# Optimization experiments

Hardware: AMD Instinct MI355X
Metric: run time of the kernel (lower is better)

The kernel has to match this reference:

```python
import jax, jax.numpy as jnp
import numpy as np

K_TOP = 2  # top-k experts per token (MoE k)


def setup_inputs() -> dict:
    key = jax.random.key(0)
    ks = jax.random.split(key, 4)
    B, D, H, E = 4096, 1024, 2048, 8
    x = jax.random.normal(ks[0], (B, D), dtype=jnp.float32)
    w_gate = jax.random.normal(ks[1], (D, E), dtype=jnp.float32) * 0.02
    W1 = jax.random.normal(ks[2], (E, D, H), dtype=jnp.float32) * (1.0 / np.sqrt(D))
    b1 = jnp.zeros((E, H), dtype=jnp.float32)
    W2 = jax.random.normal(ks[3], (E, H, D), dtype=jnp.float32) * (1.0 / np.sqrt(H))
    b2 = jnp.zeros((E, D), dtype=jnp.float32)
    return {"x": x, "w_gate": w_gate, "W1": W1, "b1": b1, "W2": W2, "b2": b2}


def _top_k_gates(logits, k):
    # noisy_top_k_gating, eval path (noisy_gating=False / train=False):
    # softmax over the top-k logits, scattered back to [B, E]; other gates are 0.
    B, E = logits.shape
    top_logits, top_idx = jax.lax.top_k(logits, k)       # [B, k]
    top_gates = jax.nn.softmax(top_logits, axis=-1)      # [B, k]
    rows = jnp.arange(B)[:, None]
    gates = jnp.zeros((B, E), dtype=logits.dtype).at[rows, top_idx].set(top_gates)
    return gates


def reference(x, w_gate, W1, b1, W2, b2):
    # Gating
    logits = x @ w_gate                                  # [B, E]
    gates = _top_k_gates(logits, K_TOP)                  # [B, E], sparse (top-k nonzero)
    # Experts: MLP(fc1 -> relu -> fc2) per expert. Dense-all-experts form is
    # mathematically identical to dispatch/combine since zero gates contribute 0.
    h = jax.nn.relu(jnp.einsum('bd,edh->beh', x, W1) + b1[None])   # [B, E, H]
    y = jnp.einsum('beh,ehd->bed', h, W2) + b2[None]               # [B, E, D]
    out = jnp.einsum('be,bed->bd', gates, y)                       # gated scatter-combine
    return out
```

## Files before the change

kernel.cpp:

```cpp
#include <hip/hip_runtime.h>

#define B_TOK 4096
#define DDIM  1024
#define HDIM  2048
#define NEXP  8
#define MAXTOK 4096
#define BM 128
#define BN 128
#define BK 32

#define OFF_W1T  0ull
#define OFF_W2T  33554432ull
#define OFF_XB   67108864ull
#define OFF_H    75497472ull
#define OFF_Y    109051904ull
#define OFF_TOK  125829120ull
#define OFF_GATE 125960192ull
#define OFF_PAIR 126091264ull
#define OFF_CNT  126124032ull
#define OFF_OFFS 126124096ull
#define OFF_EIDX (OFF_Y)
#define OFF_GCO  (OFF_Y + 16384ull)

typedef __attribute__((ext_vector_type(4))) float f32x4;
typedef __attribute__((ext_vector_type(8))) short bf16x8;

static __device__ __forceinline__ unsigned short f2bf(float f) {
    unsigned u = __builtin_bit_cast(unsigned, f);
    unsigned r = (u + 0x7FFFu + ((u >> 16) & 1u)) >> 16;
    return (unsigned short)r;
}
static __device__ __forceinline__ float bf2f(unsigned short s) {
    unsigned u = ((unsigned)s) << 16;
    return __builtin_bit_cast(float, u);
}

#define AS1(p) ((const __attribute__((address_space(1))) void*)(p))
#define AS3(p) ((__attribute__((address_space(3))) void*)(p))

__global__ void __launch_bounds__(256) gating_logits_kernel(
    const float* __restrict__ x, const float* __restrict__ wg,
    int* __restrict__ eidx, float* __restrict__ gco) {
    int wave = threadIdx.x >> 6;
    int lane = threadIdx.x & 63;
    int b = blockIdx.x * 4 + wave;
    float acc[NEXP];
#pragma unroll
    for (int e = 0; e < NEXP; e++) acc[e] = 0.f;
    const float* xr = x + (size_t)b * DDIM;
#pragma unroll
    for (int i = 0; i < DDIM / 64; i++) {
        int d = i * 64 + lane;
        float xv = xr[d];
        const float4* wrow = (const float4*)(wg + (size_t)d * NEXP);
        float4 w0 = wrow[0], w1 = wrow[1];
        acc[0] += xv * w0.x; acc[1] += xv * w0.y; acc[2] += xv * w0.z; acc[3] += xv * w0.w;
        acc[4] += xv * w1.x; acc[5] += xv * w1.y; acc[6] += xv * w1.z; acc[7] += xv * w1.w;
    }
#pragma unroll
    for (int off = 32; off >= 1; off >>= 1)
#pragma unroll
        for (int e = 0; e < NEXP; e++) acc[e] += __shfl_xor(acc[e], off);
    if (lane == 0) {
        int i1 = 0; float m1 = acc[0];
        for (int e = 1; e < NEXP; e++) if (acc[e] > m1) { m1 = acc[e]; i1 = e; }
        int i2 = (i1 == 0) ? 1 : 0; float m2 = -1e30f;
        for (int e = 0; e < NEXP; e++) { if (e == i1) continue; if (acc[e] > m2) { m2 = acc[e]; i2 = e; } }
        float g1 = 1.f / (1.f + expf(m2 - m1));
        eidx[b] = i1 | (i2 << 16);
        gco[b] = g1;
    }
}

__global__ void __launch_bounds__(256) build_kernel(
    const int* __restrict__ eidx, const float* __restrict__ gco,
    int* __restrict__ counts, int* __restrict__ tok,
    float* __restrict__ gate, int* __restrict__ pair) {
    __shared__ int lhist[NEXP];
    __shared__ int gbase[NEXP];
    int t = threadIdx.x;
    if (t < NEXP) lhist[t] = 0;
    __syncthreads();
    int b = blockIdx.x * 256 + t;
    int ep = eidx[b];
    int e1 = ep & 0xffff, e2 = ep >> 16;
    float g1 = gco[b], g2 = 1.f - g1;
    int l1 = atomicAdd(&lhist[e1], 1);
    int l2 = atomicAdd(&lhist[e2], 1);
    __syncthreads();
    if (t < NEXP) gbase[t] = atomicAdd(&counts[t], lhist[t]);
    __syncthreads();
    int s1 = gbase[e1] + l1, s2 = gbase[e2] + l2;
    tok[e1 * MAXTOK + s1] = b; gate[e1 * MAXTOK + s1] = g1; pair[b * 2 + 0] = e1 * MAXTOK + s1;
    tok[e2 * MAXTOK + s2] = b; gate[e2 * MAXTOK + s2] = g2; pair[b * 2 + 1] = e2 * MAXTOK + s2;
}

__global__ void scan_kernel(const int* __restrict__ counts, int* __restrict__ offs) {
    if (threadIdx.x == 0) {
        int s = 0;
        for (int e = 0; e < NEXP; e++) { offs[e] = s; s += counts[e]; }
    }
}

__global__ void __launch_bounds__(256) cvtx_kernel(const float* __restrict__ src, short* __restrict__ dst) {
    int i = blockIdx.x * 256 + threadIdx.x;
    float4 v = ((const float4*)src)[i];
    short4 o;
    o.x = (short)f2bf(v.x); o.y = (short)f2bf(v.y);
    o.z = (short)f2bf(v.z); o.w = (short)f2bf(v.w);
    ((short4*)dst)[i] = o;
}

__global__ void __launch_bounds__(256) tcvt_kernel(const float* __restrict__ src, short* __restrict__ dst,
                                                   int R, int C) {
    __shared__ float tile[64][65];
    int e = blockIdx.z;
    size_t base = (size_t)e * R * C;
    int r0 = blockIdx.y * 64, c0 = blockIdx.x * 64;
    int t = threadIdx.x;
    int rr = t >> 4, c4 = (t & 15) * 4;
    const float* s = src + base + (size_t)r0 * C + c0;
#pragma unroll
    for (int i = 0; i < 4; i++) {
        float4 v = *(const float4*)(s + (size_t)(rr + i * 16) * C + c4);
        tile[rr + i * 16][c4 + 0] = v.x; tile[rr + i * 16][c4 + 1] = v.y;
        tile[rr + i * 16][c4 + 2] = v.z; tile[rr + i * 16][c4 + 3] = v.w;
    }
    __syncthreads();
    short* d = dst + base + (size_t)c0 * R + r0;
    int hr0 = t >> 4, dc = (t & 15) * 4;
#pragma unroll
    for (int i = 0; i < 4; i++) {
        int hr = hr0 + i * 16;
        short4 o;
        o.x = (short)f2bf(tile[dc + 0][hr]); o.y = (short)f2bf(tile[dc + 1][hr]);
        o.z = (short)f2bf(tile[dc + 2][hr]); o.w = (short)f2bf(tile[dc + 3][hr]);
        *(short4*)(d + (size_t)hr * R + dc) = o;
    }
}

__global__ void __launch_bounds__(256) fc1_kernel(
    const short* __restrict__ Xb, const short* __restrict__ W1T, const float* __restrict__ b1,
    short* __restrict__ h, const int* __restrict__ tok,
    const int* __restrict__ counts, const int* __restrict__ offs) {
    int e = blockIdx.z;
    int cnt = counts[e];
    int m0 = blockIdx.y * BM;
    if (m0 >= cnt) return;
    int n0 = blockIdx.x * BN;
    int baseh = offs[e];

    __shared__ short As[BM * BK];
    __shared__ short Bs[BN * BK];

    int t = threadIdx.x;
    int wave = t >> 6, lane = t & 63;

    const short* asrc[2]; short* adst[2];
    const short* bsrc[2]; short* bdst[2];
#pragma unroll
    for (int i = 0; i < 2; i++) {
        int e0 = wave * 512 + i * 2048 + lane * 8;
        int r = e0 >> 5, ck = e0 & 31;
        int trow = m0 + r;
        int tid2 = (trow < cnt) ? tok[e * MAXTOK + trow] : 0;
        asrc[i] = Xb + (size_t)tid2 * DDIM + ck;
        adst[i] = As + wave * 512 + i * 2048;
        bsrc[i] = W1T + ((size_t)e * HDIM + n0 + r) * DDIM + ck;
        bdst[i] = Bs + wave * 512 + i * 2048;
    }

    int wr = (wave >> 1) * 64, wc = (wave & 1) * 64;
    f32x4 acc[4][4];
    f32x4 zero = {0.f, 0.f, 0.f, 0.f};
#pragma unroll
    for (int m = 0; m < 4; m++)
#pragma unroll
        for (int n = 0; n < 4; n++) acc[m][n] = zero;

    int aoff[4], boff[4];
#pragma unroll
    for (int m = 0; m < 4; m++) aoff[m] = (wr + m * 16 + (lane & 15)) * BK + (lane >> 4) * 8;
#pragma unroll
    for (int n = 0; n < 4; n++) boff[n] = (wc + n * 16 + (lane & 15)) * BK + (lane >> 4) * 8;

    for (int kt = 0; kt < DDIM / BK; kt++) {
        int k0 = kt * BK;
        __builtin_amdgcn_global_load_lds(AS1(asrc[0] + k0), AS3(adst[0]), 16, 0, 0);
        __builtin_amdgcn_global_load_lds(AS1(asrc[1] + k0), AS3(adst[1]), 16, 0, 0);
        __builtin_amdgcn_global_load_lds(AS1(bsrc[0] + k0), AS3(bdst[0]), 16, 0, 0);
        __builtin_amdgcn_global_load_lds(AS1(bsrc[1] + k0), AS3(bdst[1]), 16, 0, 0);
        __syncthreads();
        bf16x8 af[4], bg[4];
#pragma unroll
        for (int m = 0; m < 4; m++) af[m] = *(const bf16x8*)(As + aoff[m]);
#pragma unroll
        for (int n = 0; n < 4; n++) bg[n] = *(const bf16x8*)(Bs + boff[n]);
#pragma unroll
        for (int m = 0; m < 4; m++)
#pragma unroll
            for (int n = 0; n < 4; n++)
                acc[m][n] = __builtin_amdgcn_mfma_f32_16x16x32_bf16(af[m], bg[n], acc[m][n], 0, 0, 0);
        __syncthreads();
    }

#pragma unroll
    for (int n = 0; n < 4; n++) {
        int col = n0 + wc + n * 16 + (lane & 15);
        float bias = b1[e * HDIM + col];
#pragma unroll
        for (int m = 0; m < 4; m++) {
            int rbase = wr + m * 16 + (lane >> 4) * 4;
#pragma unroll
            for (int j = 0; j < 4; j++) {
                int r = rbase + j;
                if (m0 + r < cnt) {
                    float v = acc[m][n][j] + bias;
                    v = v > 0.f ? v : 0.f;
                    h[(size_t)(baseh + m0 + r) * HDIM + col] = (short)f2bf(v);
                }
            }
        }
    }
}

__global__ void __launch_bounds__(256) fc2_kernel(
    const short* __restrict__ h, const short* __restrict__ W2T, const float* __restrict__ b2,
    short* __restrict__ ybuf, const int* __restrict__ counts, const int* __restrict__ offs) {
    int e = blockIdx.z;
    int cnt = counts[e];
    int m0 = blockIdx.y * BM;
    if (m0 >= cnt) return;
    int n0 = blockIdx.x * BN;
    int baseh = offs[e];

    __shared__ short As[BM * BK];
    __shared__ short Bs[BN * BK];

    int t = threadIdx.x;
    int wave = t >> 6, lane = t & 63;

    const short* asrc[2]; short* adst[2];
    const short* bsrc[2]; short* bdst[2];
#pragma unroll
    for (int i = 0; i < 2; i++) {
        int e0 = wave * 512 + i * 2048 + lane * 8;
        int r = e0 >> 5, ck = e0 & 31;
        asrc[i] = h + (size_t)(baseh + m0 + r) * HDIM + ck;
        adst[i] = As + wave * 512 + i * 2048;
        bsrc[i] = W2T + ((size_t)e * DDIM + n0 + r) * HDIM + ck;
        bdst[i] = Bs + wave * 512 + i * 2048;
    }

    int wr = (wave >> 1) * 64, wc = (wave & 1) * 64;
    f32x4 acc[4][4];
    f32x4 zero = {0.f, 0.f, 0.f, 0.f};
#pragma unroll
    for (int m = 0; m < 4; m++)
#pragma unroll
        for (int n = 0; n < 4; n++) acc[m][n] = zero;

    int aoff[4], boff[4];
#pragma unroll
    for (int m = 0; m < 4; m++) aoff[m] = (wr + m * 16 + (lane & 15)) * BK + (lane >> 4) * 8;
#pragma unroll
    for (int n = 0; n < 4; n++) boff[n] = (wc + n * 16 + (lane & 15)) * BK + (lane >> 4) * 8;

    for (int kt = 0; kt < HDIM / BK; kt++) {
        int k0 = kt * BK;
        __builtin_amdgcn_global_load_lds(AS1(asrc[0] + k0), AS3(adst[0]), 16, 0, 0);
        __builtin_amdgcn_global_load_lds(AS1(asrc[1] + k0), AS3(adst[1]), 16, 0, 0);
        __builtin_amdgcn_global_load_lds(AS1(bsrc[0] + k0), AS3(bdst[0]), 16, 0, 0);
        __builtin_amdgcn_global_load_lds(AS1(bsrc[1] + k0), AS3(bdst[1]), 16, 0, 0);
        __syncthreads();
        bf16x8 af[4], bg[4];
#pragma unroll
        for (int m = 0; m < 4; m++) af[m] = *(const bf16x8*)(As + aoff[m]);
#pragma unroll
        for (int n = 0; n < 4; n++) bg[n] = *(const bf16x8*)(Bs + boff[n]);
#pragma unroll
        for (int m = 0; m < 4; m++)
#pragma unroll
            for (int n = 0; n < 4; n++)
                acc[m][n] = __builtin_amdgcn_mfma_f32_16x16x32_bf16(af[m], bg[n], acc[m][n], 0, 0, 0);
        __syncthreads();
    }

#pragma unroll
    for (int n = 0; n < 4; n++) {
        int col = n0 + wc + n * 16 + (lane & 15);
        float bias = b2[e * DDIM + col];
#pragma unroll
        for (int m = 0; m < 4; m++) {
            int rbase = wr + m * 16 + (lane >> 4) * 4;
#pragma unroll
            for (int j = 0; j < 4; j++) {
                int r = rbase + j;
                if (m0 + r < cnt) {
                    float v = acc[m][n][j] + bias;
                    ybuf[(size_t)(baseh + m0 + r) * DDIM + col] = (short)f2bf(v);
                }
            }
        }
    }
}

__global__ void __launch_bounds__(256) combine_kernel(
    const short* __restrict__ ybuf, const float* __restrict__ gate,
    const int* __restrict__ pair, const int* __restrict__ offs, float* __restrict__ out) {
    int b = blockIdx.x;
    int p0 = pair[b * 2], p1 = pair[b * 2 + 1];
    float g0 = gate[p0], g1 = gate[p1];
    int r0 = offs[p0 >> 12] + (p0 & 4095);
    int r1 = offs[p1 >> 12] + (p1 & 4095);
    const short4* y0 = (const short4*)(ybuf + (size_t)r0 * DDIM);
    const short4* y1 = (const short4*)(ybuf + (size_t)r1 * DDIM);
    float4* o = (float4*)(out + (size_t)b * DDIM);
    int t = threadIdx.x;
    short4 a = y0[t], c = y1[t];
    float4 v;
    v.x = g0 * bf2f((unsigned short)a.x) + g1 * bf2f((unsigned short)c.x);
    v.y = g0 * bf2f((unsigned short)a.y) + g1 * bf2f((unsigned short)c.y);
    v.z = g0 * bf2f((unsigned short)a.z) + g1 * bf2f((unsigned short)c.z);
    v.w = g0 * bf2f((unsigned short)a.w) + g1 * bf2f((unsigned short)c.w);
    o[t] = v;
}

extern "C" void kernel_launch(void* const* d_in, const int* in_sizes, int n_in,
                              void* d_out, int out_size, void* d_ws, size_t ws_size,
                              hipStream_t stream) {
    const float* x  = (const float*)d_in[0];
    const float* wg = (const float*)d_in[1];
    const float* W1 = (const float*)d_in[2];
    const float* b1 = (const float*)d_in[3];
    const float* W2 = (const float*)d_in[4];
    const float* b2 = (const float*)d_in[5];
    float* out = (float*)d_out;
    char* ws = (char*)d_ws;

    short* W1T = (short*)(ws + OFF_W1T);
    short* W2T = (short*)(ws + OFF_W2T);
    short* Xb  = (short*)(ws + OFF_XB);
    short* h   = (short*)(ws + OFF_H);
    short* ybuf = (short*)(ws + OFF_Y);
    int* tok   = (int*)(ws + OFF_TOK);
    float* gate = (float*)(ws + OFF_GATE);
    int* pair  = (int*)(ws + OFF_PAIR);
    int* counts = (int*)(ws + OFF_CNT);
    int* offs  = (int*)(ws + OFF_OFFS);
    int* eidx  = (int*)(ws + OFF_EIDX);
    float* gco = (float*)(ws + OFF_GCO);

    hipMemsetAsync(counts, 0, 64, stream);
    gating_logits_kernel<<<B_TOK / 4, 256, 0, stream>>>(x, wg, eidx, gco);
    build_kernel<<<B_TOK / 256, 256, 0, stream>>>(eidx, gco, counts, tok, gate, pair);
    scan_kernel<<<1, 64, 0, stream>>>(counts, offs);
    cvtx_kernel<<<(B_TOK * DDIM / 4) / 256, 256, 0, stream>>>(x, Xb);
    tcvt_kernel<<<dim3(HDIM / 64, DDIM / 64, NEXP), 256, 0, stream>>>(W1, W1T, DDIM, HDIM);
    tcvt_kernel<<<dim3(DDIM / 64, HDIM / 64, NEXP), 256, 0, stream>>>(W2, W2T, HDIM, DDIM);
    fc1_kernel<<<dim3(HDIM / BN, MAXTOK / BM, NEXP), 256, 0, stream>>>(Xb, W1T, b1, h, tok, counts, offs);
    fc2_kernel<<<dim3(DDIM / BN, MAXTOK / BM, NEXP), 256, 0, stream>>>(h, W2T, b2, ybuf, counts, offs);
    combine_kernel<<<B_TOK, 256, 0, stream>>>(ybuf, gate, pair, offs, out);
}
```

Before: 211.5 us.

## Double-buffer expert GEMM LDS tiles, swizzle LDS, fuse x conversion into gating

Both expert GEMM kernels now use two LDS buffers per operand. The next K-tile's global-to-LDS load is issued before the current tile's MFMAs, which removes one barrier per iteration and overlaps memory with compute. LDS rows use an XOR swizzle on the 8-element chunks to cut bank conflicts. Swapping the MFMA operands transposes the output layout, so the epilogue writes short4 vectors with float4 bias loads. The separate x-to-bf16 conversion kernel is folded into the gating kernel to save a launch and a pass over x, though the fused stores are scalar 2-byte writes. LDS use doubles, which may lower occupancy.

```diff
diff --git a/kernel.cpp b/kernel.cpp
--- a/kernel.cpp
+++ b/kernel.cpp
@@ -40,7 +40,7 @@
 
 __global__ void __launch_bounds__(256) gating_logits_kernel(
     const float* __restrict__ x, const float* __restrict__ wg,
-    int* __restrict__ eidx, float* __restrict__ gco) {
+    int* __restrict__ eidx, float* __restrict__ gco, short* __restrict__ Xb) {
     int wave = threadIdx.x >> 6;
     int lane = threadIdx.x & 63;
     int b = blockIdx.x * 4 + wave;
@@ -48,10 +48,12 @@
 #pragma unroll
     for (int e = 0; e < NEXP; e++) acc[e] = 0.f;
     const float* xr = x + (size_t)b * DDIM;
+    short* xbr = Xb + (size_t)b * DDIM;
 #pragma unroll
     for (int i = 0; i < DDIM / 64; i++) {
         int d = i * 64 + lane;
         float xv = xr[d];
+        xbr[d] = (short)f2bf(xv);
         const float4* wrow = (const float4*)(wg + (size_t)d * NEXP);
         float4 w0 = wrow[0], w1 = wrow[1];
         acc[0] += xv * w0.x; acc[1] += xv * w0.y; acc[2] += xv * w0.z; acc[3] += xv * w0.w;
@@ -100,15 +102,6 @@
         int s = 0;
         for (int e = 0; e < NEXP; e++) { offs[e] = s; s += counts[e]; }
     }
-}
-
-__global__ void __launch_bounds__(256) cvtx_kernel(const float* __restrict__ src, short* __restrict__ dst) {
-    int i = blockIdx.x * 256 + threadIdx.x;
-    float4 v = ((const float4*)src)[i];
-    short4 o;
-    o.x = (short)f2bf(v.x); o.y = (short)f2bf(v.y);
-    o.z = (short)f2bf(v.z); o.w = (short)f2bf(v.w);
-    ((short4*)dst)[i] = o;
 }
 
 __global__ void __launch_bounds__(256) tcvt_kernel(const float* __restrict__ src, short* __restrict__ dst,
@@ -150,25 +143,25 @@
     int n0 = blockIdx.x * BN;
     int baseh = offs[e];
 
-    __shared__ short As[BM * BK];
-    __shared__ short Bs[BN * BK];
+    __shared__ short As[2][BM * BK];
+    __shared__ short Bs[2][BN * BK];
 
     int t = threadIdx.x;
     int wave = t >> 6, lane = t & 63;
 
-    const short* asrc[2]; short* adst[2];
-    const short* bsrc[2]; short* bdst[2];
+    const short* asrc[2]; const short* bsrc[2];
 #pragma unroll
     for (int i = 0; i < 2; i++) {
         int e0 = wave * 512 + i * 2048 + lane * 8;
-        int r = e0 >> 5, ck = e0 & 31;
+        int r = e0 >> 5;
+        int q = (e0 >> 3) & 3;
+        int cks = ((q ^ (r & 3)) << 3);
         int trow = m0 + r;
         int tid2 = (trow < cnt) ? tok[e * MAXTOK + trow] : 0;
-        asrc[i] = Xb + (size_t)tid2 * DDIM + ck;
-        adst[i] = As + wave * 512 + i * 2048;
-        bsrc[i] = W1T + ((size_t)e * HDIM + n0 + r) * DDIM + ck;
-        bdst[i] = Bs + wave * 512 + i * 2048;
-    }
+        asrc[i] = Xb + (size_t)tid2 * DDIM + cks;
+        bsrc[i] = W1T + ((size_t)e * HDIM + n0 + r) * DDIM + cks;
+    }
+    int d0 = wave * 512, d1 = wave * 512 + 2048;
 
     int wr = (wave >> 1) * 64, wc = (wave & 1) * 64;
     f32x4 acc[4][4];
@@ -178,47 +171,72 @@
 #pragma unroll
         for (int n = 0; n < 4; n++) acc[m][n] = zero;
 
+    int qsw = (((lane >> 4) ^ (lane & 3)) << 3);
     int aoff[4], boff[4];
 #pragma unroll
-    for (int m = 0; m < 4; m++) aoff[m] = (wr + m * 16 + (lane & 15)) * BK + (lane >> 4) * 8;
-#pragma unroll
-    for (int n = 0; n < 4; n++) boff[n] = (wc + n * 16 + (lane & 15)) * BK + (lane >> 4) * 8;
-
-    for (int kt = 0; kt < DDIM / BK; kt++) {
-        int k0 = kt * BK;
-        __builtin_amdgcn_global_load_lds(AS1(asrc[0] + k0), AS3(adst[0]), 16, 0, 0);
-        __builtin_amdgcn_global_load_lds(AS1(asrc[1] + k0), AS3(adst[1]), 16, 0, 0);
-        __builtin_amdgcn_global_load_lds(AS1(bsrc[0] + k0), AS3(bdst[0]), 16, 0, 0);
-        __builtin_amdgcn_global_load_lds(AS1(bsrc[1] + k0), AS3(bdst[1]), 16, 0, 0);
+    for (int m = 0; m < 4; m++) aoff[m] = (wr + m * 16 + (lane & 15)) * BK + qsw;
+#pragma unroll
+    for (int n = 0; n < 4; n++) boff[n] = (wc + n * 16 + (lane & 15)) * BK + qsw;
+
+#define STAGE1(buf, k0) do { \
+    __builtin_amdgcn_global_load_lds(AS1(asrc[0] + (k0)), AS3(&As[buf][d0]), 16, 0, 0); \
+    __builtin_amdgcn_global_load_lds(AS1(asrc[1] + (k0)), AS3(&As[buf][d1]), 16, 0, 0); \
+    __builtin_amdgcn_global_load_lds(AS1(bsrc[0] + (k0)), AS3(&Bs[buf][d0]), 16, 0, 0); \
+    __builtin_amdgcn_global_load_lds(AS1(bsrc[1] + (k0)), AS3(&Bs[buf][d1]), 16, 0, 0); \
+} while (0)
+
+    STAGE1(0, 0);
+    __syncthreads();
+    int cur = 0;
+    const int NT = DDIM / BK;
+    for (int kt = 0; kt < NT - 1; ++kt) {
+        STAGE1(cur ^ 1, (kt + 1) * BK);
+        bf16x8 af[4], bg[4];
+#pragma unroll
+        for (int m = 0; m < 4; m++) af[m] = *(const bf16x8*)(&As[cur][aoff[m]]);
+#pragma unroll
+        for (int n = 0; n < 4; n++) bg[n] = *(const bf16x8*)(&Bs[cur][boff[n]]);
+        __builtin_amdgcn_s_setprio(1);
+#pragma unroll
+        for (int m = 0; m < 4; m++)
+#pragma unroll
+            for (int n = 0; n < 4; n++)
+                acc[m][n] = __builtin_amdgcn_mfma_f32_16x16x32_bf16(bg[n], af[m], acc[m][n], 0, 0, 0);
+        __builtin_amdgcn_s_setprio(0);
         __syncthreads();
+        cur ^= 1;
+    }
+    {
         bf16x8 af[4], bg[4];
 #pragma unroll
-        for (int m = 0; m < 4; m++) af[m] = *(const bf16x8*)(As + aoff[m]);
-#pragma unroll
-        for (int n = 0; n < 4; n++) bg[n] = *(const bf16x8*)(Bs + boff[n]);
+        for (int m = 0; m < 4; m++) af[m] = *(const bf16x8*)(&As[cur][aoff[m]]);
+#pragma unroll
+        for (int n = 0; n < 4; n++) bg[n] = *(const bf16x8*)(&Bs[cur][boff[n]]);
 #pragma unroll
         for (int m = 0; m < 4; m++)
 #pragma unroll
             for (int n = 0; n < 4; n++)
-                acc[m][n] = __builtin_amdgcn_mfma_f32_16x16x32_bf16(af[m], bg[n], acc[m][n], 0, 0, 0);
-        __syncthreads();
-    }
-
-#pragma unroll
-    for (int n = 0; n < 4; n++) {
-        int col = n0 + wc + n * 16 + (lane & 15);
-        float bias = b1[e * HDIM + col];
-#pragma unroll
-        for (int m = 0; m < 4; m++) {
-            int rbase = wr + m * 16 + (lane >> 4) * 4;
-#pragma unroll
-            for (int j = 0; j < 4; j++) {
-                int r = rbase + j;
-                if (m0 + r < cnt) {
-                    float v = acc[m][n][j] + bias;
-                    v = v > 0.f ? v : 0.f;
-                    h[(size_t)(baseh + m0 + r) * HDIM + col] = (short)f2bf(v);
-                }
+                acc[m][n] = __builtin_amdgcn_mfma_f32_16x16x32_bf16(bg[n], af[m], acc[m][n], 0, 0, 0);
+    }
+#undef STAGE1
+
+#pragma unroll
+    for (int m = 0; m < 4; m++) {
+        int row = m0 + wr + m * 16 + (lane & 15);
+        if (row < cnt) {
+            size_t rb = (size_t)(baseh + row) * HDIM;
+#pragma unroll
+            for (int n = 0; n < 4; n++) {
+                int colb = n0 + wc + n * 16 + ((lane >> 4) << 2);
+                float4 bias = *(const float4*)(b1 + e * HDIM + colb);
+                float v0 = acc[m][n][0] + bias.x; v0 = v0 > 0.f ? v0 : 0.f;
+                float v1 = acc[m][n][1] + bias.y; v1 = v1 > 0.f ? v1 : 0.f;
+                float v2 = acc[m][n][2] + bias.z; v2 = v2 > 0.f ? v2 : 0.f;
+                float v3 = acc[m][n][3] + bias.w; v3 = v3 > 0.f ? v3 : 0.f;
+                short4 o;
+                o.x = (short)f2bf(v0); o.y = (short)f2bf(v1);
+                o.z = (short)f2bf(v2); o.w = (short)f2bf(v3);
+                *(short4*)(h + rb + colb) = o;
             }
         }
     }
@@ -234,23 +252,23 @@
     int n0 = blockIdx.x * BN;
     int baseh = offs[e];
 
-    __shared__ short As[BM * BK];
-    __shared__ short Bs[BN * BK];
+    __shared__ short As[2][BM * BK];
+    __shared__ short Bs[2][BN * BK];
 
     int t = threadIdx.x;
     int wave = t >> 6, lane = t & 63;
 
-    const short* asrc[2]; short* adst[2];
-    const short* bsrc[2]; short* bdst[2];
+    const short* asrc[2]; const short* bsrc[2];
 #pragma unroll
     for (int i = 0; i < 2; i++) {
         int e0 = wave * 512 + i * 2048 + lane * 8;
-        int r = e0 >> 5, ck = e0 & 31;
-        asrc[i] = h + (size_t)(baseh + m0 + r) * HDIM + ck;
-        adst[i] = As + wave * 512 + i * 2048;
-        bsrc[i] = W2T + ((size_t)e * DDIM + n0 + r) * HDIM + ck;
-        bdst[i] = Bs + wave * 512 + i * 2048;
-    }
+        int r = e0 >> 5;
+        int q = (e0 >> 3) & 3;
+        int cks = ((q ^ (r & 3)) << 3);
+        asrc[i] = h + (size_t)(baseh + m0 + r) * HDIM + cks;
+        bsrc[i] = W2T + ((size_t)e * DDIM + n0 + r) * HDIM + cks;
+    }
+    int d0 = wave * 512, d1 = wave * 512 + 2048;
 
     int wr = (wave >> 1) * 64, wc = (wave & 1) * 64;
     f32x4 acc[4][4];
@@ -260,46 +278,70 @@
 #pragma unroll
         for (int n = 0; n < 4; n++) acc[m][n] = zero;
 
+    int qsw = (((lane >> 4) ^ (lane & 3)) << 3);
     int aoff[4], boff[4];
 #pragma unroll
-    for (int m = 0; m < 4; m++) aoff[m] = (wr + m * 16 + (lane & 15)) * BK + (lane >> 4) * 8;
-#pragma unroll
-    for (int n = 0; n < 4; n++) boff[n] = (wc + n * 16 + (lane & 15)) * BK + (lane >> 4) * 8;
-
-    for (int kt = 0; kt < HDIM / BK; kt++) {
-        int k0 = kt * BK;
-        __builtin_amdgcn_global_load_lds(AS1(asrc[0] + k0), AS3(adst[0]), 16, 0, 0);
-        __builtin_amdgcn_global_load_lds(AS1(asrc[1] + k0), AS3(adst[1]), 16, 0, 0);
-        __builtin_amdgcn_global_load_lds(AS1(bsrc[0] + k0), AS3(bdst[0]), 16, 0, 0);
-        __builtin_amdgcn_global_load_lds(AS1(bsrc[1] + k0), AS3(bdst[1]), 16, 0, 0);
+    for (int m = 0; m < 4; m++) aoff[m] = (wr + m * 16 + (lane & 15)) * BK + qsw;
+#pragma unroll
+    for (int n = 0; n < 4; n++) boff[n] = (wc + n * 16 + (lane & 15)) * BK + qsw;
+
+#define STAGE2(buf, k0) do { \
+    __builtin_amdgcn_global_load_lds(AS1(asrc[0] + (k0)), AS3(&As[buf][d0]), 16, 0, 0); \
+    __builtin_amdgcn_global_load_lds(AS1(asrc[1] + (k0)), AS3(&As[buf][d1]), 16, 0, 0); \
+    __builtin_amdgcn_global_load_lds(AS1(bsrc[0] + (k0)), AS3(&Bs[buf][d0]), 16, 0, 0); \
+    __builtin_amdgcn_global_load_lds(AS1(bsrc[1] + (k0)), AS3(&Bs[buf][d1]), 16, 0, 0); \
+} while (0)
+
+    STAGE2(0, 0);
+    __syncthreads();
+    int cur = 0;
+    const int NT = HDIM / BK;
+    for (int kt = 0; kt < NT - 1; ++kt) {
+        STAGE2(cur ^ 1, (kt + 1) * BK);
+        bf16x8 af[4], bg[4];
+#pragma unroll
+        for (int m = 0; m < 4; m++) af[m] = *(const bf16x8*)(&As[cur][aoff[m]]);
+#pragma unroll
+        for (int n = 0; n < 4; n++) bg[n] = *(const bf16x8*)(&Bs[cur][boff[n]]);
+        __builtin_amdgcn_s_setprio(1);
+#pragma unroll
+        for (int m = 0; m < 4; m++)
+#pragma unroll
+            for (int n = 0; n < 4; n++)
+                acc[m][n] = __builtin_amdgcn_mfma_f32_16x16x32_bf16(bg[n], af[m], acc[m][n], 0, 0, 0);
+        __builtin_amdgcn_s_setprio(0);
         __syncthreads();
+        cur ^= 1;
+    }
+    {
         bf16x8 af[4], bg[4];
 #pragma unroll
-        for (int m = 0; m < 4; m++) af[m] = *(const bf16x8*)(As + aoff[m]);
-#pragma unroll
-        for (int n = 0; n < 4; n++) bg[n] = *(const bf16x8*)(Bs + boff[n]);
+        for (int m = 0; m < 4; m++) af[m] = *(const bf16x8*)(&As[cur][aoff[m]]);
+#pragma unroll
+        for (int n = 0; n < 4; n++) bg[n] = *(const bf16x8*)(&Bs[cur][boff[n]]);
 #pragma unroll
         for (int m = 0; m < 4; m++)
 #pragma unroll
             for (int n = 0; n < 4; n++)
-                acc[m][n] = __builtin_amdgcn_mfma_f32_16x16x32_bf16(af[m], bg[n], acc[m][n], 0, 0, 0);
-        __syncthreads();
-    }
-
-#pragma unroll
-    for (int n = 0; n < 4; n++) {
-        int col = n0 + wc + n * 16 + (lane & 15);
-        float bias = b2[e * DDIM + col];
-#pragma unroll
-        for (int m = 0; m < 4; m++) {
-            int rbase = wr + m * 16 + (lane >> 4) * 4;
-#pragma unroll
-            for (int j = 0; j < 4; j++) {
-                int r = rbase + j;
-                if (m0 + r < cnt) {
-                    float v = acc[m][n][j] + bias;
-                    ybuf[(size_t)(baseh + m0 + r) * DDIM + col] = (short)f2bf(v);
-                }
+                acc[m][n] = __builtin_amdgcn_mfma_f32_16x16x32_bf16(bg[n], af[m], acc[m][n], 0, 0, 0);
+    }
+#undef STAGE2
+
+#pragma unroll
+    for (int m = 0; m < 4; m++) {
+        int row = m0 + wr + m * 16 + (lane & 15);
+        if (row < cnt) {
+            size_t rb = (size_t)(baseh + row) * DDIM;
+#pragma unroll
+            for (int n = 0; n < 4; n++) {
+                int colb = n0 + wc + n * 16 + ((lane >> 4) << 2);
+                float4 bias = *(const float4*)(b2 + e * DDIM + colb);
+                short4 o;
+                o.x = (short)f2bf(acc[m][n][0] + bias.x);
+                o.y = (short)f2bf(acc[m][n][1] + bias.y);
+                o.z = (short)f2bf(acc[m][n][2] + bias.z);
+                o.w = (short)f2bf(acc[m][n][3] + bias.w);
+                *(short4*)(ybuf + rb + colb) = o;
             }
         }
     }
@@ -352,10 +394,9 @@
     float* gco = (float*)(ws + OFF_GCO);
 
     hipMemsetAsync(counts, 0, 64, stream);
-    gating_logits_kernel<<<B_TOK / 4, 256, 0, stream>>>(x, wg, eidx, gco);
+    gating_logits_kernel<<<B_TOK / 4, 256, 0, stream>>>(x, wg, eidx, gco, Xb);
     build_kernel<<<B_TOK / 256, 256, 0, stream>>>(eidx, gco, counts, tok, gate, pair);
     scan_kernel<<<1, 64, 0, stream>>>(counts, offs);
-    cvtx_kernel<<<(B_TOK * DDIM / 4) / 256, 256, 0, stream>>>(x, Xb);
     tcvt_kernel<<<dim3(HDIM / 64, DDIM / 64, NEXP), 256, 0, stream>>>(W1, W1T, DDIM, HDIM);
     tcvt_kernel<<<dim3(DDIM / 64, HDIM / 64, NEXP), 256, 0, stream>>>(W2, W2T, HDIM, DDIM);
     fc1_kernel<<<dim3(HDIM / BN, MAXTOK / BM, NEXP), 256, 0, stream>>>(Xb, W1T, b1, h, tok, counts, offs);
```

New measurement: 201.8 us. 4.6% less time.
